# Optimization experiments

Hardware: AMD Instinct MI355X
Metric: run time of the kernel (lower is better)

## Reference

```python
import jax, jax.numpy as jnp
import numpy as np

B, S, V, E, H = 256, 64, 30000, 300, 512
D_A, R, C, P = 350, 8, 150, 16
NUM_ITERS = 3
EPS = 1e-9


def _xavier(k, shape, fi, fo):
    lim = (6.0 / (fi + fo)) ** 0.5
    return jax.random.uniform(k, shape, minval=-lim, maxval=lim, dtype=jnp.float32)


def setup_inputs() -> dict:
    key = jax.random.key(0)
    ks = jax.random.split(key, 14)
    u = 1.0 / (H ** 0.5)
    uni = lambda k, shp: jax.random.uniform(k, shp, minval=-u, maxval=u, dtype=jnp.float32)
    return {
        'input_x': jax.random.randint(ks[0], (B, S), 0, V, dtype=jnp.int32),
        'lens': jnp.full((B,), S, dtype=jnp.int32),
        'embedding': jax.random.normal(ks[1], (V, E), dtype=jnp.float32) * 0.1,
        'w_ih_f': uni(ks[2], (4 * H, E)), 'w_hh_f': uni(ks[3], (4 * H, H)),
        'b_ih_f': uni(ks[4], (4 * H,)), 'b_hh_f': uni(ks[5], (4 * H,)),
        'w_ih_b': uni(ks[6], (4 * H, E)), 'w_hh_b': uni(ks[7], (4 * H, H)),
        'b_ih_b': uni(ks[8], (4 * H,)), 'b_hh_b': uni(ks[9], (4 * H,)),
        'ws1': _xavier(ks[10], (D_A, 2 * H), 2 * H, D_A),
        'ws2': _xavier(ks[11], (R, D_A), D_A, R),
        'capsule_weights': _xavier(ks[12], (R, 2 * H, C * P), 2 * H, C * P),
    }


def _lstm_dir(x, w_ih, w_hh, b_ih, b_hh, reverse):
    # x: [S, B, E] -> hidden states [S, B, H] (torch gate order i, f, g, o)
    b = x.shape[1]
    def step(carry, xt):
        h, c = carry
        z = xt @ w_ih.T + h @ w_hh.T + (b_ih + b_hh)
        i, f, g, o = jnp.split(z, 4, axis=-1)
        c = jax.nn.sigmoid(f) * c + jax.nn.sigmoid(i) * jnp.tanh(g)
        h = jax.nn.sigmoid(o) * jnp.tanh(c)
        return (h, c), h
    init = (jnp.zeros((b, H), x.dtype), jnp.zeros((b, H), x.dtype))
    _, hs = jax.lax.scan(step, init, x, reverse=reverse)
    return hs


def _squash(s):
    # tool.squash: (|s|^2 / (1+|s|^2)) * s / |s|
    n2 = jnp.sum(s * s, axis=-1, keepdims=True)
    return (n2 / (1.0 + n2)) * s / jnp.sqrt(n2 + EPS)


def _forward(input_x, embedding, w_ih_f, w_hh_f, b_ih_f, b_hh_f,
             w_ih_b, w_hh_b, b_ih_b, b_hh_b, ws1, ws2, capsule_weights):
    # embed; torch transposes [B,S] -> [S,B] then embeds -> [S,B,E]
    emb = embedding[input_x.T]
    # bidirectional LSTM (lens == S, so pack/pad is identity)
    h_fwd = _lstm_dir(emb, w_ih_f, w_hh_f, b_ih_f, b_hh_f, reverse=False)
    h_bwd = _lstm_dir(emb, w_ih_b, w_hh_b, b_ih_b, b_hh_b, reverse=True)
    output = jnp.transpose(jnp.concatenate([h_fwd, h_bwd], axis=-1), (1, 0, 2))  # [B,S,2H]
    # structured self-attention (dropout is identity at p=0 / eval)
    pre = jnp.tanh(jnp.einsum('bsd,ad->bsa', output, ws1))          # [B,S,d_a]
    att = jnp.einsum('bsa,ra->brs', pre, ws2)                        # [B,r,S]
    attention = jax.nn.softmax(att, axis=-1)
    semantic = jnp.einsum('brs,bsd->brd', attention, output)         # [B,r,2H]
    # prediction vectors: sum_d semantic[b,r,d] * W[r,d,k]
    pred = jnp.einsum('brd,rdk->brk', semantic, capsule_weights)
    pred = pred.reshape(-1, R, C, P)                                 # [B,r,C,P]
    # dynamic routing
    logits = jnp.zeros((pred.shape[0], R, C), pred.dtype)
    routes = None
    v = None
    for _ in range(NUM_ITERS):
        routes = jax.nn.softmax(logits, axis=2)                      # [B,r,C]
        preact = jnp.einsum('brc,brcp->bcp', routes, pred)           # [B,C,P]
        v = _squash(preact)
        logits = logits + jnp.einsum('brcp,bcp->brc', pred, v)
    class_logits = jnp.linalg.norm(v, axis=-1)                       # [B,C]
    return attention, class_logits, pred, routes


def reference(input_x, lens, embedding, w_ih_f, w_hh_f, b_ih_f, b_hh_f,
              w_ih_b, w_hh_b, b_ih_b, b_hh_b, ws1, ws2, capsule_weights):
    del lens  # all lengths == S: pack/pad identity
    return _forward(input_x, embedding, w_ih_f, w_hh_f, b_ih_f, b_hh_f,
                    w_ih_b, w_hh_b, b_ih_b, b_hh_b, ws1, ws2, capsule_weights)
```

## Files before the change

### kernel.cpp

```cpp
#include <hip/hip_runtime.h>
#include <hip/hip_bf16.h>
#include <hip/hip_cooperative_groups.h>
#include <math.h>

#define BB 256
#define SS 64
#define EE 300
#define EPX 320
#define KP 832
#define VV 30000
#define HH 512
#define H2 1024
#define DA 350
#define RR 8
#define CC 150
#define PP 16
#define CP 2400
#define NPF 4096

#define ATT_OFF    0L
#define CL_OFF     131072L
#define PRED_OFF   169472L
#define ROUTES_OFF 5084672L

typedef _Float16 f16;
typedef f16  f16x8 __attribute__((ext_vector_type(8)));
typedef f16  f16x4 __attribute__((ext_vector_type(4)));
typedef float f32x4 __attribute__((ext_vector_type(4)));

static __device__ __forceinline__ float sigmN(float x) { return 1.0f / (1.0f + expf(-x)); }

#define NG_ ((long)SS * BB * EPX)
#define NW_ ((long)2 * 2048 * KP)
#define NS_ ((long)384 * 1024)
__global__ __launch_bounds__(256) void n_stage(
    const int* __restrict__ ids, const float* __restrict__ emb,
    const float* __restrict__ wihF, const float* __restrict__ whhF,
    const float* __restrict__ wihB, const float* __restrict__ whhB,
    const float* __restrict__ ws1,
    f16* __restrict__ X16, f16* __restrict__ W16, f16* __restrict__ ws1_16,
    unsigned* __restrict__ pflag)
{
    const long idx = (long)blockIdx.x * 256 + threadIdx.x;
    if (idx < NG_) {
        const int e = (int)(idx % EPX);
        const int row = (int)(idx / EPX);
        const int s = row >> 8, b = row & 255;
        int tok = ids[(long)b * SS + s];
        if ((unsigned)tok >= (unsigned)VV) tok = 0;
        X16[idx] = (e < EE) ? (f16)emb[(long)tok * EE + e] : (f16)0.0f;
    } else if (idx < NG_ + NW_) {
        const long i2 = idx - NG_;
        const int dir = (int)(i2 / (2048 * KP));
        const int rem = (int)(i2 % (2048 * KP));
        const int j = rem / KP, k = rem % KP;
        const float* wih = dir ? wihB : wihF;
        const float* whh = dir ? whhB : whhF;
        float v;
        if (k < EE)        v = wih[(long)j * EE + k];
        else if (k < EPX)  v = 0.0f;
        else               v = whh[(long)j * HH + (k - EPX)];
        W16[i2] = (f16)v;
    } else if (idx < NG_ + NW_ + NS_) {
        const long i3 = idx - NG_ - NW_;
        const int j = (int)(i3 >> 10);
        ws1_16[i3] = (j < DA) ? (f16)ws1[i3] : (f16)0.0f;
    } else if (idx < NG_ + NW_ + NS_ + NPF) {
        pflag[idx - NG_ - NW_ - NS_] = 0u;
    }
}

__global__ __launch_bounds__(256) void n_packcapsT(
    const float* __restrict__ caps, f16* __restrict__ capsT)
{
    __shared__ float t[32][33];
    const int r = blockIdx.z, k0 = blockIdx.x * 32, n0 = blockIdx.y * 32;
    const int tx = threadIdx.x & 31, ty = threadIdx.x >> 5;
    #pragma unroll
    for (int p = 0; p < 4; ++p) {
        const int k = k0 + ty + p * 8;
        const int n = n0 + tx;
        t[ty + p * 8][tx] = (n < CP) ? caps[((long)r * H2 + k) * CP + n] : 0.0f;
    }
    __syncthreads();
    #pragma unroll
    for (int p = 0; p < 4; ++p) {
        const int n = n0 + ty + p * 8;
        if (n < 2432)
            capsT[((long)r * 2432 + n) * H2 + k0 + tx] = (f16)t[tx][ty + p * 8];
    }
}

__global__ __launch_bounds__(512, 1) void p_lstm8(
    const f16* __restrict__ X16, f16* __restrict__ hs16,
    f16* __restrict__ hx, unsigned* __restrict__ pflag,
    const f16* __restrict__ W16,
    const float* __restrict__ bihF, const float* __restrict__ bhhF,
    const float* __restrict__ bihB, const float* __restrict__ bhhB)
{
    __shared__ f16 Wl[4 * 26 * 64 * 8];
    __shared__ f32x4 part[4][4][64];
    __shared__ f16 hstage[64][16];

    const int bid = blockIdx.x;
    const int dir = bid & 1;
    const int bq  = (bid >> 1) & 3;
    const int ut  = bid >> 3;
    const int u0  = ut * 16;
    const int b0  = bq * 64;
    const int tid = threadIdx.x;
    const int wave = tid >> 6, lane = tid & 63;
    const int bt = wave & 3, kh = wave >> 2;
    const int l15 = lane & 15;
    const int kgrp = (lane >> 4) * 8;
    const int grp32 = (dir * 4 + bq) * 32;
    unsigned* myflag = pflag + (grp32 + ut) * 16;

    {
        const f16* Wsrc = W16 + (long)dir * 2048 * KP;
        for (int f = tid; f < 4 * 26 * 64; f += 512) {
            const int g  = f / (26 * 64);
            const int rm = f % (26 * 64);
            const int kt = rm >> 6, ln = rm & 63;
            const long src = ((long)g * HH + u0 + (ln & 15)) * KP + kt * 32 + ((ln >> 4) * 8);
            *(f16x8*)(Wl + (long)f * 8) = *(const f16x8*)(Wsrc + src);
        }
    }
    __syncthreads();

    const int arow = b0 + bt * 16 + l15;
    const int u = u0 + l15;
    const float* bi = dir ? bihB : bihF;
    const float* bh = dir ? bhhB : bhhF;
    const float bias0 = bi[u]          + bh[u];
    const float bias1 = bi[HH + u]     + bh[HH + u];
    const float bias2 = bi[2 * HH + u] + bh[2 * HH + u];
    const float bias3 = bi[3 * HH + u] + bh[3 * HH + u];
    const int rbase = (lane >> 4) * 4;
    float cc[4] = {0.f, 0.f, 0.f, 0.f};

    f32x4 xacc[4];
    const int xb = kh ? 5 : 0;
    auto computeX = [&](int se) {
        #pragma unroll
        for (int g = 0; g < 4; ++g) xacc[g] = (f32x4){0.f, 0.f, 0.f, 0.f};
        const f16* Xrow = X16 + ((long)se * BB + arow) * EPX;
        #pragma unroll
        for (int j = 0; j < 5; ++j) {
            const int kt = xb + j;
            const int k0 = kt * 32 + kgrp;
            const f16x8 afr = *(const f16x8*)(Xrow + k0);
            #pragma unroll
            for (int g = 0; g < 4; ++g) {
                const f16x8 bfr = *(const f16x8*)(Wl + (((g * 26 + kt) << 6) + lane) * 8);
                xacc[g] = __builtin_amdgcn_mfma_f32_16x16x32_f16(afr, bfr, xacc[g], 0, 0, 0);
            }
        }
    };
    computeX(dir ? (SS - 1) : 0);

    const int hb = kh ? 8 : 0;
    for (int s = 0; s < SS; ++s) {
        const int s_eff = dir ? (SS - 1 - s) : s;

        if (s > 0) {
            if (wave == 0) {
                const unsigned* fp = pflag + (grp32 + (lane & 31)) * 16;
                int guard = 0;
                unsigned v = __hip_atomic_load(fp, __ATOMIC_RELAXED,
                                               __HIP_MEMORY_SCOPE_AGENT);
                while (!__all((int)(v >= (unsigned)s))) {
                    __builtin_amdgcn_s_sleep(1);
                    v = __hip_atomic_load(fp, __ATOMIC_RELAXED,
                                          __HIP_MEMORY_SCOPE_AGENT);
                    if (++guard > (1 << 22)) break;
                }
            }
            __syncthreads();
        }

        f32x4 acc[4];
        #pragma unroll
        for (int g = 0; g < 4; ++g) acc[g] = xacc[g];

        if (s > 0) {
            const f16* hrow = hx + ((((long)((s - 1) & 1) * 2 + dir) * BB) + arow) * HH;
            #pragma unroll
            for (int j = 0; j < 8; ++j) {
                const int kt = 10 + hb + j;
                const int hk = (hb + j) * 32 + kgrp;
                union { unsigned long long q[2]; f16x8 v; } uu;
                const unsigned long long* hp = (const unsigned long long*)(hrow + hk);
                uu.q[0] = __hip_atomic_load(hp,     __ATOMIC_RELAXED, __HIP_MEMORY_SCOPE_AGENT);
                uu.q[1] = __hip_atomic_load(hp + 1, __ATOMIC_RELAXED, __HIP_MEMORY_SCOPE_AGENT);
                #pragma unroll
                for (int g = 0; g < 4; ++g) {
                    const f16x8 bfr = *(const f16x8*)(Wl + (((g * 26 + kt) << 6) + lane) * 8);
                    acc[g] = __builtin_amdgcn_mfma_f32_16x16x32_f16(uu.v, bfr, acc[g], 0, 0, 0);
                }
            }
        }

        if (kh == 1) {
            #pragma unroll
            for (int g = 0; g < 4; ++g) part[bt][g][lane] = acc[g];
        }
        __syncthreads();
        if (kh == 0) {
            #pragma unroll
            for (int g = 0; g < 4; ++g) acc[g] += part[bt][g][lane];
            #pragma unroll
            for (int i = 0; i < 4; ++i) {
                const float zi = acc[0][i] + bias0;
                const float zf = acc[1][i] + bias1;
                const float zg = acc[2][i] + bias2;
                const float zo = acc[3][i] + bias3;
                cc[i] = sigmN(zf) * cc[i] + sigmN(zi) * tanhf(zg);
                hstage[bt * 16 + rbase + i][l15] = (f16)(sigmN(zo) * tanhf(cc[i]));
            }
        }
        __syncthreads();

        {
            f16* hxw = hx + (((long)(s & 1) * 2 + dir) * BB) * HH;
            if (tid < 256) {
                const int row = tid >> 2, ch = tid & 3;
                union { unsigned long long q; f16 h4[4]; } pk;
                pk.h4[0] = hstage[row][ch * 4 + 0];
                pk.h4[1] = hstage[row][ch * 4 + 1];
                pk.h4[2] = hstage[row][ch * 4 + 2];
                pk.h4[3] = hstage[row][ch * 4 + 3];
                __hip_atomic_store(
                    (unsigned long long*)(hxw + (long)(b0 + row) * HH + u0 + ch * 4),
                    pk.q, __ATOMIC_RELAXED, __HIP_MEMORY_SCOPE_AGENT);
            }
            asm volatile("s_waitcnt vmcnt(0)" ::: "memory");
        }
        __syncthreads();
        if (tid == 0)
            __hip_atomic_store(myflag, (unsigned)(s + 1),
                               __ATOMIC_RELAXED, __HIP_MEMORY_SCOPE_AGENT);

        if (tid < 256) {
            const int row = tid >> 2, ch = tid & 3;
            union { unsigned long long q; f16 h4[4]; } pk;
            pk.h4[0] = hstage[row][ch * 4 + 0];
            pk.h4[1] = hstage[row][ch * 4 + 1];
            pk.h4[2] = hstage[row][ch * 4 + 2];
            pk.h4[3] = hstage[row][ch * 4 + 3];
            *(unsigned long long*)(hs16 + ((long)(b0 + row) * SS + s_eff) * H2
                                   + dir * HH + u0 + ch * 4) = pk.q;
        }

        if (s + 1 < SS) computeX(dir ? (SS - 2 - s) : (s + 1));
    }
}

__global__ __launch_bounds__(256) void n_preG(
    const f16* __restrict__ hs16, const f16* __restrict__ ws1_16,
    f16* __restrict__ pre16)
{
    const int n0 = blockIdx.x * 192;
    const int m0 = blockIdx.y * 64;
    const int tid = threadIdx.x;
    const int wave = tid >> 6, lane = tid & 63;
    const int l15 = lane & 15;
    const int kgrp = (lane >> 4) * 8;
    const f16* Arow = hs16 + (long)(m0 + wave * 16 + l15) * H2;

    f32x4 acc[12];
    #pragma unroll
    for (int nt = 0; nt < 12; ++nt) acc[nt] = (f32x4){0.f, 0.f, 0.f, 0.f};

    for (int kt = 0; kt < 32; ++kt) {
        const int k0 = kt * 32 + kgrp;
        const f16x8 afr = *(const f16x8*)(Arow + k0);
        #pragma unroll
        for (int nt = 0; nt < 12; ++nt) {
            const f16x8 bfr = *(const f16x8*)(ws1_16 + (long)(n0 + nt * 16 + l15) * H2 + k0);
            acc[nt] = __builtin_amdgcn_mfma_f32_16x16x32_f16(afr, bfr, acc[nt], 0, 0, 0);
        }
    }

    const int rbase = (lane >> 4) * 4;
    #pragma unroll
    for (int nt = 0; nt < 12; ++nt) {
        const int n = n0 + nt * 16 + l15;
        if (n < DA) {
            #pragma unroll
            for (int i = 0; i < 4; ++i) {
                const int m = m0 + wave * 16 + rbase + i;
                pre16[(long)m * DA + n] = (f16)tanhf(acc[nt][i]);
            }
        }
    }
}

__global__ __launch_bounds__(256) void n_attsem(
    const f16* __restrict__ pre16, const float* __restrict__ ws2,
    const f16* __restrict__ hs16,
    float* __restrict__ att_out, f16* __restrict__ sem16)
{
    __shared__ f16 preS[SS * DA];
    __shared__ float w2S[RR * DA];
    __shared__ float logS[RR * SS];
    __shared__ float aS[RR * SS];
    __shared__ float rmax[RR], rsum[RR];
    const int b = blockIdx.x, tid = threadIdx.x;
    {
        const unsigned long long* src =
            (const unsigned long long*)(pre16 + (long)b * SS * DA);
        unsigned long long* dst = (unsigned long long*)preS;
        for (int i = tid; i < SS * DA / 4; i += 256) dst[i] = src[i];
    }
    for (int i = tid; i < RR * DA; i += 256) w2S[i] = ws2[i];
    __syncthreads();
    for (int pp = tid; pp < RR * SS; pp += 256) {
        const int r = pp >> 6, s = pp & 63;
        const f16* prow = &preS[s * DA];
        const float* wrow = &w2S[r * DA];
        float a = 0.0f;
        for (int k = 0; k < DA; ++k) a = fmaf((float)prow[k], wrow[k], a);
        logS[r * SS + s] = a;
    }
    __syncthreads();
    if (tid < RR) {
        float mx = -1e30f;
        for (int s = 0; s < SS; ++s) mx = fmaxf(mx, logS[tid * SS + s]);
        float sm = 0.0f;
        for (int s = 0; s < SS; ++s) sm += expf(logS[tid * SS + s] - mx);
        rmax[tid] = mx; rsum[tid] = sm;
    }
    __syncthreads();
    for (int pp = tid; pp < RR * SS; pp += 256) {
        const int r = pp >> 6;
        const float v = expf(logS[pp] - rmax[r]) / rsum[r];
        att_out[(long)b * RR * SS + pp] = v;
        aS[pp] = v;
    }
    __syncthreads();

    const int d0 = tid * 4;
    float acc[RR][4] = {};
    const f16* hb = hs16 + (long)b * SS * H2;
    for (int s = 0; s < SS; ++s) {
        const f16x4 hv = *(const f16x4*)(hb + s * H2 + d0);
        const float h0 = hv[0], h1 = hv[1], h2 = hv[2], h3 = hv[3];
        #pragma unroll
        for (int r = 0; r < RR; ++r) {
            const float a = aS[r * SS + s];
            acc[r][0] = fmaf(a, h0, acc[r][0]);
            acc[r][1] = fmaf(a, h1, acc[r][1]);
            acc[r][2] = fmaf(a, h2, acc[r][2]);
            acc[r][3] = fmaf(a, h3, acc[r][3]);
        }
    }
    #pragma unroll
    for (int r = 0; r < RR; ++r) {
        f16x4 o; o[0] = (f16)acc[r][0]; o[1] = (f16)acc[r][1];
        o[2] = (f16)acc[r][2]; o[3] = (f16)acc[r][3];
        *(f16x4*)(sem16 + ((long)b * RR + r) * H2 + d0) = o;
    }
}

__global__ __launch_bounds__(512) void n_predG(
    const f16* __restrict__ sem16, const f16* __restrict__ capsT16,
    float* __restrict__ pred_out)
{
    const int n0 = blockIdx.x * 64;
    const int r  = blockIdx.y;
    const int tid = threadIdx.x;
    const int wave = tid >> 6, lane = tid & 63;
    const int l15 = lane & 15;
    const int kgrp = (lane >> 4) * 8;
    const f16* Bp = capsT16 + (long)r * 2432 * H2;
    const f16* A0 = sem16 + ((long)(wave * 32 + l15) * RR + r) * H2;

    f32x4 acc[2][4];
    #pragma unroll
    for (int mt = 0; mt < 2; ++mt)
        #pragma unroll
        for (int nt = 0; nt < 4; ++nt) acc[mt][nt] = (f32x4){0.f, 0.f, 0.f, 0.f};

    for (int kt = 0; kt < 32; ++kt) {
        const int k0 = kt * 32 + kgrp;
        const f16x8 a0 = *(const f16x8*)(A0 + k0);
        const f16x8 a1 = *(const f16x8*)(A0 + (long)16 * RR * H2 + k0);
        #pragma unroll
        for (int nt = 0; nt < 4; ++nt) {
            const f16x8 bfr = *(const f16x8*)(Bp + (long)(n0 + nt * 16 + l15) * H2 + k0);
            acc[0][nt] = __builtin_amdgcn_mfma_f32_16x16x32_f16(a0, bfr, acc[0][nt], 0, 0, 0);
            acc[1][nt] = __builtin_amdgcn_mfma_f32_16x16x32_f16(a1, bfr, acc[1][nt], 0, 0, 0);
        }
    }

    const int rbase = (lane >> 4) * 4;
    #pragma unroll
    for (int mt = 0; mt < 2; ++mt) {
        #pragma unroll
        for (int nt = 0; nt < 4; ++nt) {
            const int n = n0 + nt * 16 + l15;
            if (n < CP) {
                #pragma unroll
                for (int i = 0; i < 4; ++i) {
                    const int m = wave * 32 + mt * 16 + rbase + i;
                    pred_out[((long)m * RR + r) * CP + n] = acc[mt][nt][i];
                }
            }
        }
    }
}

__global__ __launch_bounds__(512) void n_route(
    const float* __restrict__ pred,
    float* __restrict__ cls_out, float* __restrict__ routes_out)
{
    __shared__ float predS[RR * CP];
    __shared__ float logitS[RR * CC];
    __shared__ float routeS[RR * CC];
    __shared__ float preactS[CP];
    __shared__ float vS[CP];
    __shared__ float scaleS[CC];
    __shared__ float rmax[RR], rsum[RR];
    const int b = blockIdx.x, tid = threadIdx.x;
    const float* ps = pred + (long)b * RR * CP;
    for (int i = tid; i < RR * CP; i += 512) predS[i] = ps[i];
    for (int i = tid; i < RR * CC; i += 512) logitS[i] = 0.0f;
    __syncthreads();

    for (int it = 0; it < 3; ++it) {
        if (tid < RR) {
            float mx = -1e30f;
            for (int c = 0; c < CC; ++c) mx = fmaxf(mx, logitS[tid * CC + c]);
            float sm = 0.0f;
            for (int c = 0; c < CC; ++c) sm += expf(logitS[tid * CC + c] - mx);
            rmax[tid] = mx; rsum[tid] = sm;
        }
        __syncthreads();
        for (int i = tid; i < RR * CC; i += 512) {
            const int r = i / CC;
            routeS[i] = expf(logitS[i] - rmax[r]) / rsum[r];
        }
        __syncthreads();
        for (int cp = tid; cp < CP; cp += 512) {
            const int c = cp >> 4;
            float a = 0.0f;
            #pragma unroll
            for (int r = 0; r < RR; ++r)
                a = fmaf(routeS[r * CC + c], predS[r * CP + cp], a);
            preactS[cp] = a;
        }
        __syncthreads();
        for (int c = tid; c < CC; c += 512) {
            float n2 = 0.0f;
            #pragma unroll
            for (int p = 0; p < PP; ++p) { const float x = preactS[c * PP + p]; n2 = fmaf(x, x, n2); }
            scaleS[c] = (n2 / (1.0f + n2)) / sqrtf(n2 + 1e-9f);
        }
        __syncthreads();
        for (int cp = tid; cp < CP; cp += 512) vS[cp] = preactS[cp] * scaleS[cp >> 4];
        __syncthreads();
        for (int i = tid; i < RR * CC; i += 512) {
            const int r = i / CC, c = i % CC;
            float a = 0.0f;
            #pragma unroll
            for (int p = 0; p < PP; ++p)
                a = fmaf(predS[r * CP + c * PP + p], vS[c * PP + p], a);
            logitS[i] += a;
        }
        __syncthreads();
    }

    for (int i = tid; i < RR * CC; i += 512)
        routes_out[(long)b * RR * CC + i] = routeS[i];
    for (int c = tid; c < CC; c += 512) {
        float n2 = 0.0f;
        #pragma unroll
        for (int p = 0; p < PP; ++p) { const float x = vS[c * PP + p]; n2 = fmaf(x, x, n2); }
        cls_out[(long)b * CC + c] = sqrtf(n2);
    }
}

extern "C" void kernel_launch(void* const* d_in, const int* in_sizes, int n_in,
                              void* d_out, int out_size, void* d_ws, size_t ws_size,
                              hipStream_t stream)
{
    (void)in_sizes; (void)n_in; (void)out_size;
    const int*   ids   = (const int*)d_in[0];
    const float* emb   = (const float*)d_in[2];
    const float* wih_f = (const float*)d_in[3];
    const float* whh_f = (const float*)d_in[4];
    const float* bih_f = (const float*)d_in[5];
    const float* bhh_f = (const float*)d_in[6];
    const float* wih_b = (const float*)d_in[7];
    const float* whh_b = (const float*)d_in[8];
    const float* bih_b = (const float*)d_in[9];
    const float* bhh_b = (const float*)d_in[10];
    const float* ws1   = (const float*)d_in[11];
    const float* ws2   = (const float*)d_in[12];
    const float* caps  = (const float*)d_in[13];
    float* out = (float*)d_out;

    float* ws = (float*)d_ws;
    f16*  hs16   = (f16*)ws;
    f16*  hx     = (f16*)(ws + 8388608);
    f16*  X16    = (f16*)(ws + 8650752);
    f16*  W16    = (f16*)(ws + 11272192);
    f16*  ws1_16 = (f16*)(ws + 12976128);
    f16*  sem16  = (f16*)(ws + 13172736);
    unsigned* pflag = (unsigned*)(ws + 14221312);
    f16*  pre16  = X16;
    f16*  capsT16 = (f16*)ws;
    const size_t need = (size_t)(14221312 + NPF) * 4;
    if (ws_size < need) return;

    {
        const long total = NG_ + NW_ + NS_ + NPF;
        n_stage<<<(int)((total + 255) / 256), 256, 0, stream>>>(
            ids, emb, wih_f, whh_f, wih_b, whh_b, ws1, X16, W16, ws1_16, pflag);
    }

    {
        const f16* a0 = X16; f16* a1 = hs16; f16* a2 = hx; unsigned* a3 = pflag;
        const f16* a4 = W16;
        const float* a5 = bih_f; const float* a6 = bhh_f;
        const float* a7 = bih_b; const float* a8 = bhh_b;
        void* kargs[] = {(void*)&a0, (void*)&a1, (void*)&a2, (void*)&a3, (void*)&a4,
                         (void*)&a5, (void*)&a6, (void*)&a7, (void*)&a8};
        hipLaunchCooperativeKernel((void*)p_lstm8, dim3(256), dim3(512),
                                   kargs, 0, stream);
    }

    n_preG<<<dim3(2, 256), 256, 0, stream>>>(hs16, ws1_16, pre16);

    n_attsem<<<BB, 256, 0, stream>>>(pre16, ws2, hs16, out + ATT_OFF, sem16);

    n_packcapsT<<<dim3(32, 76, 8), 256, 0, stream>>>(caps, capsT16);

    n_predG<<<dim3(38, 8), 512, 0, stream>>>(sem16, capsT16, out + PRED_OFF);

    n_route<<<BB, 512, 0, stream>>>(out + PRED_OFF, out + CL_OFF, out + ROUTES_OFF);
}
```

Baseline: 782.4 us.

## Per-wave h publish with counter flags; retile preG/predG and widen attsem

The LSTM step now has each of the four gate-finishing waves publish its own slice of h and atomically increment the block flag. Waiters spin until the flag reaches 4*s, which removes one block-wide barrier and the single-thread flag store from the recurrent critical path. Separately, preG and predG use narrower N tiles with twice as many blocks, and attsem moves to 512 threads with fp16 dot2 for the score dot products. The ws2 weights are now rounded to fp16, which adds some precision loss, and the finer tiles reload the A operand more often.

```diff
diff --git a/kernel.cpp b/kernel.cpp
--- a/kernel.cpp
+++ b/kernel.cpp
@@ -26,14 +26,15 @@
 typedef _Float16 f16;
 typedef f16  f16x8 __attribute__((ext_vector_type(8)));
 typedef f16  f16x4 __attribute__((ext_vector_type(4)));
+typedef f16  f16x2 __attribute__((ext_vector_type(2)));
 typedef float f32x4 __attribute__((ext_vector_type(4)));
 
-static __device__ __forceinline__ float sigmN(float x) { return 1.0f / (1.0f + expf(-x)); }
+static __device__ __forceinline__ float sigmQ(float x) { return 1.0f / (1.0f + expf(-x)); }
 
 #define NG_ ((long)SS * BB * EPX)
 #define NW_ ((long)2 * 2048 * KP)
 #define NS_ ((long)384 * 1024)
-__global__ __launch_bounds__(256) void n_stage(
+__global__ __launch_bounds__(256) void q_stage(
     const int* __restrict__ ids, const float* __restrict__ emb,
     const float* __restrict__ wihF, const float* __restrict__ whhF,
     const float* __restrict__ wihB, const float* __restrict__ whhB,
@@ -70,7 +71,7 @@
     }
 }
 
-__global__ __launch_bounds__(256) void n_packcapsT(
+__global__ __launch_bounds__(256) void q_packcapsT(
     const float* __restrict__ caps, f16* __restrict__ capsT)
 {
     __shared__ float t[32][33];
@@ -91,7 +92,7 @@
     }
 }
 
-__global__ __launch_bounds__(512, 1) void p_lstm8(
+__global__ __launch_bounds__(512, 1) void p_lstm9(
     const f16* __restrict__ X16, f16* __restrict__ hs16,
     f16* __restrict__ hx, unsigned* __restrict__ pflag,
     const f16* __restrict__ W16,
@@ -166,10 +167,11 @@
         if (s > 0) {
             if (wave == 0) {
                 const unsigned* fp = pflag + (grp32 + (lane & 31)) * 16;
+                const unsigned target = 4u * (unsigned)s;
                 int guard = 0;
                 unsigned v = __hip_atomic_load(fp, __ATOMIC_RELAXED,
                                                __HIP_MEMORY_SCOPE_AGENT);
-                while (!__all((int)(v >= (unsigned)s))) {
+                while (!__all((int)(v >= target))) {
                     __builtin_amdgcn_s_sleep(1);
                     v = __hip_atomic_load(fp, __ATOMIC_RELAXED,
                                           __HIP_MEMORY_SCOPE_AGENT);
@@ -206,6 +208,7 @@
             for (int g = 0; g < 4; ++g) part[bt][g][lane] = acc[g];
         }
         __syncthreads();
+
         if (kh == 0) {
             #pragma unroll
             for (int g = 0; g < 4; ++g) acc[g] += part[bt][g][lane];
@@ -215,39 +218,27 @@
                 const float zf = acc[1][i] + bias1;
                 const float zg = acc[2][i] + bias2;
                 const float zo = acc[3][i] + bias3;
-                cc[i] = sigmN(zf) * cc[i] + sigmN(zi) * tanhf(zg);
-                hstage[bt * 16 + rbase + i][l15] = (f16)(sigmN(zo) * tanhf(cc[i]));
+                cc[i] = sigmQ(zf) * cc[i] + sigmQ(zi) * tanhf(zg);
+                hstage[bt * 16 + rbase + i][l15] = (f16)(sigmQ(zo) * tanhf(cc[i]));
             }
-        }
-        __syncthreads();
-
-        {
-            f16* hxw = hx + (((long)(s & 1) * 2 + dir) * BB) * HH;
-            if (tid < 256) {
-                const int row = tid >> 2, ch = tid & 3;
-                union { unsigned long long q; f16 h4[4]; } pk;
-                pk.h4[0] = hstage[row][ch * 4 + 0];
-                pk.h4[1] = hstage[row][ch * 4 + 1];
-                pk.h4[2] = hstage[row][ch * 4 + 2];
-                pk.h4[3] = hstage[row][ch * 4 + 3];
-                __hip_atomic_store(
-                    (unsigned long long*)(hxw + (long)(b0 + row) * HH + u0 + ch * 4),
-                    pk.q, __ATOMIC_RELAXED, __HIP_MEMORY_SCOPE_AGENT);
-            }
-            asm volatile("s_waitcnt vmcnt(0)" ::: "memory");
-        }
-        __syncthreads();
-        if (tid == 0)
-            __hip_atomic_store(myflag, (unsigned)(s + 1),
-                               __ATOMIC_RELAXED, __HIP_MEMORY_SCOPE_AGENT);
-
-        if (tid < 256) {
-            const int row = tid >> 2, ch = tid & 3;
+            asm volatile("s_waitcnt lgkmcnt(0)" ::: "memory");
+            __builtin_amdgcn_sched_barrier(0);
+
+            const int row = bt * 16 + (lane >> 2), ch = lane & 3;
             union { unsigned long long q; f16 h4[4]; } pk;
             pk.h4[0] = hstage[row][ch * 4 + 0];
             pk.h4[1] = hstage[row][ch * 4 + 1];
             pk.h4[2] = hstage[row][ch * 4 + 2];
             pk.h4[3] = hstage[row][ch * 4 + 3];
+            __hip_atomic_store(
+                (unsigned long long*)(hx + (((long)(s & 1) * 2 + dir) * BB
+                                            + b0 + row) * HH + u0 + ch * 4),
+                pk.q, __ATOMIC_RELAXED, __HIP_MEMORY_SCOPE_AGENT);
+            asm volatile("s_waitcnt vmcnt(0)" ::: "memory");
+            if (lane == 0)
+                __hip_atomic_fetch_add(myflag, 1u, __ATOMIC_RELAXED,
+                                       __HIP_MEMORY_SCOPE_AGENT);
+
             *(unsigned long long*)(hs16 + ((long)(b0 + row) * SS + s_eff) * H2
                                    + dir * HH + u0 + ch * 4) = pk.q;
         }
@@ -256,11 +247,11 @@
     }
 }
 
-__global__ __launch_bounds__(256) void n_preG(
+__global__ __launch_bounds__(256) void q_preG(
     const f16* __restrict__ hs16, const f16* __restrict__ ws1_16,
     f16* __restrict__ pre16)
 {
-    const int n0 = blockIdx.x * 192;
+    const int n0 = blockIdx.x * 96;
     const int m0 = blockIdx.y * 64;
     const int tid = threadIdx.x;
     const int wave = tid >> 6, lane = tid & 63;
@@ -268,15 +259,15 @@
     const int kgrp = (lane >> 4) * 8;
     const f16* Arow = hs16 + (long)(m0 + wave * 16 + l15) * H2;
 
-    f32x4 acc[12];
-    #pragma unroll
-    for (int nt = 0; nt < 12; ++nt) acc[nt] = (f32x4){0.f, 0.f, 0.f, 0.f};
+    f32x4 acc[6];
+    #pragma unroll
+    for (int nt = 0; nt < 6; ++nt) acc[nt] = (f32x4){0.f, 0.f, 0.f, 0.f};
 
     for (int kt = 0; kt < 32; ++kt) {
         const int k0 = kt * 32 + kgrp;
         const f16x8 afr = *(const f16x8*)(Arow + k0);
         #pragma unroll
-        for (int nt = 0; nt < 12; ++nt) {
+        for (int nt = 0; nt < 6; ++nt) {
             const f16x8 bfr = *(const f16x8*)(ws1_16 + (long)(n0 + nt * 16 + l15) * H2 + k0);
             acc[nt] = __builtin_amdgcn_mfma_f32_16x16x32_f16(afr, bfr, acc[nt], 0, 0, 0);
         }
@@ -284,7 +275,7 @@
 
     const int rbase = (lane >> 4) * 4;
     #pragma unroll
-    for (int nt = 0; nt < 12; ++nt) {
+    for (int nt = 0; nt < 6; ++nt) {
         const int n = n0 + nt * 16 + l15;
         if (n < DA) {
             #pragma unroll
@@ -296,13 +287,13 @@
     }
 }
 
-__global__ __launch_bounds__(256) void n_attsem(
+__global__ __launch_bounds__(512) void q_attsem(
     const f16* __restrict__ pre16, const float* __restrict__ ws2,
     const f16* __restrict__ hs16,
     float* __restrict__ att_out, f16* __restrict__ sem16)
 {
     __shared__ f16 preS[SS * DA];
-    __shared__ float w2S[RR * DA];
+    __shared__ f16 w2f[RR * DA];
     __shared__ float logS[RR * SS];
     __shared__ float aS[RR * SS];
     __shared__ float rmax[RR], rsum[RR];
@@ -311,16 +302,17 @@
         const unsigned long long* src =
             (const unsigned long long*)(pre16 + (long)b * SS * DA);
         unsigned long long* dst = (unsigned long long*)preS;
-        for (int i = tid; i < SS * DA / 4; i += 256) dst[i] = src[i];
-    }
-    for (int i = tid; i < RR * DA; i += 256) w2S[i] = ws2[i];
-    __syncthreads();
-    for (int pp = tid; pp < RR * SS; pp += 256) {
-        const int r = pp >> 6, s = pp & 63;
-        const f16* prow = &preS[s * DA];
-        const float* wrow = &w2S[r * DA];
+        for (int i = tid; i < SS * DA / 4; i += 512) dst[i] = src[i];
+    }
+    for (int i = tid; i < RR * DA; i += 512) w2f[i] = (f16)ws2[i];
+    __syncthreads();
+    {
+        const int r = tid >> 6, s = tid & 63;
+        const f16x2* pv = (const f16x2*)&preS[s * DA];
+        const f16x2* wv = (const f16x2*)&w2f[r * DA];
         float a = 0.0f;
-        for (int k = 0; k < DA; ++k) a = fmaf((float)prow[k], wrow[k], a);
+        for (int k = 0; k < DA / 2; ++k)
+            a = __builtin_amdgcn_fdot2(pv[k], wv[k], a, false);
         logS[r * SS + s] = a;
     }
     __syncthreads();
@@ -332,42 +324,39 @@
         rmax[tid] = mx; rsum[tid] = sm;
     }
     __syncthreads();
-    for (int pp = tid; pp < RR * SS; pp += 256) {
-        const int r = pp >> 6;
-        const float v = expf(logS[pp] - rmax[r]) / rsum[r];
-        att_out[(long)b * RR * SS + pp] = v;
-        aS[pp] = v;
-    }
-    __syncthreads();
-
-    const int d0 = tid * 4;
-    float acc[RR][4] = {};
+    {
+        const int r = tid >> 6;
+        const float v = expf(logS[tid] - rmax[r]) / rsum[r];
+        att_out[(long)b * RR * SS + tid] = v;
+        aS[tid] = v;
+    }
+    __syncthreads();
+
+    const int d0 = tid * 2;
+    float acc[RR][2] = {};
     const f16* hb = hs16 + (long)b * SS * H2;
     for (int s = 0; s < SS; ++s) {
-        const f16x4 hv = *(const f16x4*)(hb + s * H2 + d0);
-        const float h0 = hv[0], h1 = hv[1], h2 = hv[2], h3 = hv[3];
+        const f16x2 hv = *(const f16x2*)(hb + s * H2 + d0);
+        const float h0 = hv[0], h1 = hv[1];
         #pragma unroll
         for (int r = 0; r < RR; ++r) {
             const float a = aS[r * SS + s];
             acc[r][0] = fmaf(a, h0, acc[r][0]);
             acc[r][1] = fmaf(a, h1, acc[r][1]);
-            acc[r][2] = fmaf(a, h2, acc[r][2]);
-            acc[r][3] = fmaf(a, h3, acc[r][3]);
         }
     }
     #pragma unroll
     for (int r = 0; r < RR; ++r) {
-        f16x4 o; o[0] = (f16)acc[r][0]; o[1] = (f16)acc[r][1];
-        o[2] = (f16)acc[r][2]; o[3] = (f16)acc[r][3];
-        *(f16x4*)(sem16 + ((long)b * RR + r) * H2 + d0) = o;
-    }
-}
-
-__global__ __launch_bounds__(512) void n_predG(
+        f16x2 o; o[0] = (f16)acc[r][0]; o[1] = (f16)acc[r][1];
+        *(f16x2*)(sem16 + ((long)b * RR + r) * H2 + d0) = o;
+    }
+}
+
+__global__ __launch_bounds__(512) void q_predG(
     const f16* __restrict__ sem16, const f16* __restrict__ capsT16,
     float* __restrict__ pred_out)
 {
-    const int n0 = blockIdx.x * 64;
+    const int n0 = blockIdx.x * 32;
     const int r  = blockIdx.y;
     const int tid = threadIdx.x;
     const int wave = tid >> 6, lane = tid & 63;
@@ -376,18 +365,18 @@
     const f16* Bp = capsT16 + (long)r * 2432 * H2;
     const f16* A0 = sem16 + ((long)(wave * 32 + l15) * RR + r) * H2;
 
-    f32x4 acc[2][4];
+    f32x4 acc[2][2];
     #pragma unroll
     for (int mt = 0; mt < 2; ++mt)
         #pragma unroll
-        for (int nt = 0; nt < 4; ++nt) acc[mt][nt] = (f32x4){0.f, 0.f, 0.f, 0.f};
+        for (int nt = 0; nt < 2; ++nt) acc[mt][nt] = (f32x4){0.f, 0.f, 0.f, 0.f};
 
     for (int kt = 0; kt < 32; ++kt) {
         const int k0 = kt * 32 + kgrp;
         const f16x8 a0 = *(const f16x8*)(A0 + k0);
         const f16x8 a1 = *(const f16x8*)(A0 + (long)16 * RR * H2 + k0);
         #pragma unroll
-        for (int nt = 0; nt < 4; ++nt) {
+        for (int nt = 0; nt < 2; ++nt) {
             const f16x8 bfr = *(const f16x8*)(Bp + (long)(n0 + nt * 16 + l15) * H2 + k0);
             acc[0][nt] = __builtin_amdgcn_mfma_f32_16x16x32_f16(a0, bfr, acc[0][nt], 0, 0, 0);
             acc[1][nt] = __builtin_amdgcn_mfma_f32_16x16x32_f16(a1, bfr, acc[1][nt], 0, 0, 0);
@@ -398,7 +387,7 @@
     #pragma unroll
     for (int mt = 0; mt < 2; ++mt) {
         #pragma unroll
-        for (int nt = 0; nt < 4; ++nt) {
+        for (int nt = 0; nt < 2; ++nt) {
             const int n = n0 + nt * 16 + l15;
             if (n < CP) {
                 #pragma unroll
@@ -411,7 +400,7 @@
     }
 }
 
-__global__ __launch_bounds__(512) void n_route(
+__global__ __launch_bounds__(512) void q_route(
     const float* __restrict__ pred,
     float* __restrict__ cls_out, float* __restrict__ routes_out)
 {
@@ -516,7 +505,7 @@
 
     {
         const long total = NG_ + NW_ + NS_ + NPF;
-        n_stage<<<(int)((total + 255) / 256), 256, 0, stream>>>(
+        q_stage<<<(int)((total + 255) / 256), 256, 0, stream>>>(
             ids, emb, wih_f, whh_f, wih_b, whh_b, ws1, X16, W16, ws1_16, pflag);
     }
 
@@ -527,17 +516,17 @@
         const float* a7 = bih_b; const float* a8 = bhh_b;
         void* kargs[] = {(void*)&a0, (void*)&a1, (void*)&a2, (void*)&a3, (void*)&a4,
                          (void*)&a5, (void*)&a6, (void*)&a7, (void*)&a8};
-        hipLaunchCooperativeKernel((void*)p_lstm8, dim3(256), dim3(512),
+        hipLaunchCooperativeKernel((void*)p_lstm9, dim3(256), dim3(512),
                                    kargs, 0, stream);
     }
 
-    n_preG<<<dim3(2, 256), 256, 0, stream>>>(hs16, ws1_16, pre16);
-
-    n_attsem<<<BB, 256, 0, stream>>>(pre16, ws2, hs16, out + ATT_OFF, sem16);
-
-    n_packcapsT<<<dim3(32, 76, 8), 256, 0, stream>>>(caps, capsT16);
-
-    n_predG<<<dim3(38, 8), 512, 0, stream>>>(sem16, capsT16, out + PRED_OFF);
-
-    n_route<<<BB, 512, 0, stream>>>(out + PRED_OFF, out + CL_OFF, out + ROUTES_OFF);
-}
+    q_preG<<<dim3(4, 256), 256, 0, stream>>>(hs16, ws1_16, pre16);
+
+    q_attsem<<<BB, 512, 0, stream>>>(pre16, ws2, hs16, out + ATT_OFF, sem16);
+
+    q_packcapsT<<<dim3(32, 76, 8), 256, 0, stream>>>(caps, capsT16);
+
+    q_predG<<<dim3(76, 8), 512, 0, stream>>>(sem16, capsT16, out + PRED_OFF);
+
+    q_route<<<BB, 512, 0, stream>>>(out + PRED_OFF, out + CL_OFF, out + ROUTES_OFF);
+}
```

After: 741.0 us. -5.3%, faster.
